# Performance work log

Measured on AMD Instinct MI355X. Metric: run time of the kernel, lower is better.

## Reference

```python
import jax, jax.numpy as jnp
import numpy as np

B, P, D, DOUT = 8, 4096, 512, 512
E, K, NHID = 8, 2, 2  # num_experts, top_k, num_mlp_hidden_layers
L = NHID + 1          # number of D->D (relu) layers per expert


def setup_inputs() -> dict:
    key = jax.random.key(0)
    ks = jax.random.split(key, 7)
    s_in = 1.0 / np.sqrt(D)
    s_g = 1.0 / np.sqrt(3.0)
    x = jax.random.normal(ks[0], (B, P, D), dtype=jnp.float32)
    Wg = jax.random.uniform(ks[1], (3, E), jnp.float32, -s_g, s_g)
    bg = jax.random.uniform(ks[2], (E,), jnp.float32, -s_g, s_g)
    Wh = jax.random.uniform(ks[3], (E, L, D, D), jnp.float32, -s_in, s_in)
    bh = jax.random.uniform(ks[4], (E, L, D), jnp.float32, -s_in, s_in)
    Wo = jax.random.uniform(ks[5], (E, D, DOUT), jnp.float32, -s_in, s_in)
    bo = jax.random.uniform(ks[6], (E, DOUT), jnp.float32, -s_in, s_in)
    return {"x": x, "Wg": Wg, "bg": bg, "Wh": Wh, "bh": bh, "Wo": Wo, "bo": bo}


def _moe_forward(x, Wg, bg, Wh, bh, Wo, bo):
    b, p, d = x.shape
    xf = x.reshape(-1, d)                       # [N, D]
    n = xf.shape[0]
    gates = xf[:, -3:] @ Wg + bg                # [N, E] (eval mode: no noise)
    topv, topi = jax.lax.top_k(gates, K)        # [N, K]
    topw = jax.nn.softmax(topv, axis=-1)        # [N, K]
    # scatter top-k softmax weights into dense [N, E] mask
    mask = jnp.zeros_like(gates).at[jnp.arange(n)[:, None], topi].set(topw)
    out = jnp.zeros((n, Wo.shape[-1]), dtype=xf.dtype)
    for e in range(E):  # fixed small expert loop; zero-weight rows contribute 0
        h = xf
        for l in range(L):
            h = jax.nn.relu(h @ Wh[e, l] + bh[e, l])
        y = h @ Wo[e] + bo[e]
        out = out + mask[:, e:e + 1] * y
    return out.reshape(b, p, -1)


def reference(x, Wg, bg, Wh, bh, Wo, bo):
    return _moe_forward(x, Wg, bg, Wh, bh, Wo, bo)
```

## Files before the change

### kernel.cpp

```cpp
#include <hip/hip_runtime.h>
#include <cstdint>
#include <cstddef>

#define DD   512
#define NTOK 32768
#define NE   8
#define BM   128
#define BN   128
#define BK   32
#define NT   (DD / BK)
#define RBLK 1024

typedef unsigned int  u32;
typedef unsigned short u16;
typedef unsigned long long u64;
using f16x8 = __attribute__((ext_vector_type(8))) _Float16;
using f32x4 = __attribute__((ext_vector_type(4))) float;

#define OA 0
#define OB 4096

__device__ __forceinline__ u16 f16bits(float f) {
    union { _Float16 h; u16 u; } p;
    p.h = (_Float16)f;
    return p.u;
}
__device__ __forceinline__ uint4 pack_f16x8(const float4& a, const float4& b) {
    uint4 r;
    r.x = (u32)f16bits(a.x) | ((u32)f16bits(a.y) << 16);
    r.y = (u32)f16bits(a.z) | ((u32)f16bits(a.w) << 16);
    r.z = (u32)f16bits(b.x) | ((u32)f16bits(b.y) << 16);
    r.w = (u32)f16bits(b.z) | ((u32)f16bits(b.w) << 16);
    return r;
}

__device__ __forceinline__ void gl16(const void* src, const u16* ldsdst) {
    __builtin_amdgcn_global_load_lds(
        (const __attribute__((address_space(1))) u32*)src,
        (__attribute__((address_space(3))) u32*)(void*)ldsdst, 16, 0, 0);
}

__global__ __launch_bounds__(RBLK) void route_kernel(
    const float* __restrict__ x,
    const float* __restrict__ Wg,
    const float* __restrict__ bg,
    int t0, int T,
    int* __restrict__ counts,
    int* __restrict__ eids,
    float* __restrict__ wts) {
    __shared__ int lcnt[NE];
    int tid = threadIdx.x;
    if (tid < NE) lcnt[tid] = 0;
    __syncthreads();

    int i = blockIdx.x * RBLK + tid;
    bool active = (i < T);
    int e0 = 0, e1 = 0;
    if (active) {
        int n = t0 + i;
        const float* xr = x + (size_t)n * DD + (DD - 3);
        float x0 = xr[0], x1 = xr[1], x2 = xr[2];
        float g[NE];
#pragma unroll
        for (int e = 0; e < NE; e++)
            g[e] = x0 * Wg[e] + x1 * Wg[NE + e] + x2 * Wg[2 * NE + e] + bg[e];
        float v0 = g[0];
#pragma unroll
        for (int e = 1; e < NE; e++) if (g[e] > v0) { v0 = g[e]; e0 = e; }
        float v1 = -3.0e38f; e1 = -1;
#pragma unroll
        for (int e = 0; e < NE; e++) if (e != e0 && g[e] > v1) { v1 = g[e]; e1 = e; }
        float t = expf(v1 - v0);
        float s = 1.0f / (1.0f + t);
        eids[2 * i] = e0; eids[2 * i + 1] = e1;
        wts[2 * i] = s;  wts[2 * i + 1] = t * s;
    }

    int lane = tid & 63;
#pragma unroll
    for (int k = 0; k < 2; k++) {
        int e = active ? (k ? e1 : e0) : -1;
#pragma unroll
        for (int ex = 0; ex < NE; ex++) {
            u64 m = __ballot(e == ex);
            if (m && lane == 0) atomicAdd(&lcnt[ex], __popcll(m));
        }
    }
    __syncthreads();
    if (tid < NE && lcnt[tid]) atomicAdd(&counts[tid], lcnt[tid]);
}

__global__ void offsets_kernel(const int* __restrict__ counts,
                               int* __restrict__ off,
                               int* __restrict__ cursor) {
    if (threadIdx.x == 0) {
        int acc = 0;
        for (int e = 0; e < NE; e++) {
            off[e] = acc;
            cursor[e] = acc;
            acc += (counts[e] + (BM - 1)) & ~(BM - 1);
        }
        off[NE] = acc;
    }
}

__global__ __launch_bounds__(RBLK) void scatter_kernel(
    int t0, int T,
    const int* __restrict__ eids,
    int* __restrict__ cursor,
    int* __restrict__ list_token,
    int* __restrict__ posl) {
    __shared__ int lcnt[NE], lbase[NE];
    __shared__ int woff[RBLK / 64][NE];
    int tid = threadIdx.x, lane = tid & 63, wv = tid >> 6;
    int i = blockIdx.x * RBLK + tid;
    bool active = (i < T);
    u64 lmask = (1ull << lane) - 1ull;

#pragma unroll
    for (int k = 0; k < 2; k++) {
        if (tid < NE) lcnt[tid] = 0;
        __syncthreads();
        int e = active ? eids[2 * i + k] : -1;
        u64 mymask = 0;
#pragma unroll
        for (int ex = 0; ex < NE; ex++) {
            u64 m = __ballot(e == ex);
            if (e == ex) mymask = m;
            if (m && lane == 0) woff[wv][ex] = atomicAdd(&lcnt[ex], __popcll(m));
        }
        __syncthreads();
        if (tid < NE) lbase[tid] = lcnt[tid] ? atomicAdd(&cursor[tid], lcnt[tid]) : 0;
        __syncthreads();
        if (active) {
            int p = lbase[e] + woff[wv][e] + __popcll(mymask & lmask);
            list_token[p] = t0 + i;
            posl[2 * i + k] = p;
        }
        __syncthreads();
    }
}

__global__ void convert_w(const float* __restrict__ Wh,
                          const float* __restrict__ Wo,
                          u16* __restrict__ Wt) {
    __shared__ float tile[32][33];
    int z = blockIdx.z;
    int e = z >> 2, l = z & 3;
    const float* src = (l < 3) ? (Wh + ((size_t)e * 3 + l) * DD * DD)
                               : (Wo + (size_t)e * DD * DD);
    int bx = blockIdx.x, by = blockIdx.y;
    int tx = threadIdx.x, ty = threadIdx.y;
#pragma unroll
    for (int j = 0; j < 4; j++)
        tile[ty + j * 8][tx] = src[(size_t)(by * 32 + ty + j * 8) * DD + bx * 32 + tx];
    __syncthreads();
    u16* d = Wt + (size_t)z * DD * DD;
#pragma unroll
    for (int j = 0; j < 4; j++) {
        int n = bx * 32 + ty + j * 8;
        int k = by * 32 + tx;
        d[(size_t)n * DD + k] = f16bits(tile[tx][ty + j * 8]);
    }
}

template <bool GATHER, bool RELU, bool OUTF32>
__global__ __launch_bounds__(256, 3) void moe_gemm(
    const float* __restrict__ Xf,
    const u16* __restrict__ Ain,
    const int* __restrict__ list_token,
    const u16* __restrict__ Wt,
    int layer,
    const float* __restrict__ bptr, int bestride,
    const int* __restrict__ off,
    u16* __restrict__ Ch,
    float* __restrict__ Cf)
{
    u32 nb = gridDim.x, qq = nb >> 3, bid = blockIdx.x;
    u32 wg = (bid & 7) * qq + (bid >> 3);
    int rb = (int)(wg >> 2) * BM;
    if (rb >= off[NE]) return;
    int cb = (int)(wg & 3) * BN;
    int e = 0;
#pragma unroll
    for (int s = 1; s < NE; s++) if (rb >= off[s]) e = s;

    __shared__ u16 lds[8192];

    const int tid = threadIdx.x;
    const int lane = tid & 63, wv = tid >> 6;

    int rowj[2], usj[2];
#pragma unroll
    for (int j = 0; j < 2; j++) {
        rowj[j] = j * 64 + (tid >> 2);
        usj[j]  = (tid & 3) ^ ((rowj[j] >> 1) & 3);
    }

    const size_t wbase = ((size_t)e * 4 + layer) * (size_t)DD * DD;
    const u16* bS[2];
    const u16* aS[2];
    const float* aF[2];
    int tokj[2] = {0, 0};
#pragma unroll
    for (int j = 0; j < 2; j++) {
        bS[j] = Wt + wbase + (size_t)(cb + rowj[j]) * DD + usj[j] * 8;
        if (GATHER) {
            tokj[j] = list_token[rb + rowj[j]];
            aF[j] = Xf + (size_t)(tokj[j] < 0 ? 0 : tokj[j]) * DD + usj[j] * 8;
        } else {
            aS[j] = Ain + (size_t)(rb + rowj[j]) * DD + usj[j] * 8;
        }
    }
    const int cb8[2] = { wv * 512, 2048 + wv * 512 };

    const int r15 = lane & 15, lg = lane >> 4;
    const int wr = (wv >> 1) * 64, wc = (wv & 1) * 64;
    u32 aoff[4], boff[4];
#pragma unroll
    for (int i = 0; i < 4; i++) {
        int ar = wr + i * 16 + r15;
        aoff[i] = (u32)(ar * 32 + (lg ^ ((ar >> 1) & 3)) * 8);
        int br = wc + i * 16 + r15;
        boff[i] = (u32)(br * 32 + (lg ^ ((br >> 1) & 3)) * 8);
    }

    f32x4 acc[4][4];
#pragma unroll
    for (int i = 0; i < 4; i++)
#pragma unroll
        for (int j = 0; j < 4; j++) acc[i][j] = (f32x4){0.f, 0.f, 0.f, 0.f};

    for (int t = 0; t < NT; t++) {
        const int k0 = t * BK;
#pragma unroll
        for (int j = 0; j < 2; j++)
            gl16(bS[j] + k0, &lds[OB + cb8[j]]);
        if (GATHER) {
#pragma unroll
            for (int j = 0; j < 2; j++) {
                const float4* fp = (const float4*)(aF[j] + k0);
                float4 f0 = fp[0], f1 = fp[1];
                if (tokj[j] < 0) { f0 = make_float4(0.f, 0.f, 0.f, 0.f); f1 = f0; }
                *(uint4*)&lds[OA + rowj[j] * 32 + (tid & 3) * 8] = pack_f16x8(f0, f1);
            }
        } else {
#pragma unroll
            for (int j = 0; j < 2; j++)
                gl16(aS[j] + k0, &lds[OA + cb8[j]]);
        }
        __syncthreads();

        f16x8 a[4];
#pragma unroll
        for (int mi = 0; mi < 4; mi++)
            a[mi] = *(const f16x8*)&lds[OA + aoff[mi]];
#pragma unroll
        for (int ni = 0; ni < 4; ni++) {
            f16x8 b = *(const f16x8*)&lds[OB + boff[ni]];
#pragma unroll
            for (int mi = 0; mi < 4; mi++)
                acc[mi][ni] = __builtin_amdgcn_mfma_f32_16x16x32_f16(a[mi], b, acc[mi][ni], 0, 0, 0);
        }
        __syncthreads();
    }

#pragma unroll
    for (int ni = 0; ni < 4; ni++) {
        int col = cb + wc + ni * 16 + r15;
        float bbias = bptr[e * bestride + col];
#pragma unroll
        for (int mi = 0; mi < 4; mi++) {
            int row0 = rb + wr + mi * 16 + lg * 4;
#pragma unroll
            for (int rr = 0; rr < 4; rr++) {
                float v = acc[mi][ni][rr] + bbias;
                if (RELU) v = fmaxf(v, 0.f);
                size_t idx = (size_t)(row0 + rr) * DD + col;
                if (OUTF32) Cf[idx] = v;
                else        Ch[idx] = f16bits(v);
            }
        }
    }
}

__global__ void combine_kernel(int t0, int T,
                               const float* __restrict__ y,
                               const int* __restrict__ posl,
                               const float* __restrict__ wts,
                               float* __restrict__ out) {
    int idx = blockIdx.x * blockDim.x + threadIdx.x;
    if (idx >= T * (DD / 4)) return;
    int i = idx >> 7;
    int j = idx & 127;
    int p0 = posl[2 * i], p1 = posl[2 * i + 1];
    float w0 = wts[2 * i], w1 = wts[2 * i + 1];
    float4 a = ((const float4*)(y + (size_t)p0 * DD))[j];
    float4 b = ((const float4*)(y + (size_t)p1 * DD))[j];
    float4 c;
    c.x = w0 * a.x + w1 * b.x;
    c.y = w0 * a.y + w1 * b.y;
    c.z = w0 * a.z + w1 * b.z;
    c.w = w0 * a.w + w1 * b.w;
    ((float4*)(out + (size_t)(t0 + i) * DD))[j] = c;
}

extern "C" void kernel_launch(void* const* d_in, const int* in_sizes, int n_in,
                              void* d_out, int out_size, void* d_ws, size_t ws_size,
                              hipStream_t stream) {
    const float* x  = (const float*)d_in[0];
    const float* Wg = (const float*)d_in[1];
    const float* bg = (const float*)d_in[2];
    const float* Wh = (const float*)d_in[3];
    const float* bh = (const float*)d_in[4];
    const float* Wo = (const float*)d_in[5];
    const float* bo = (const float*)d_in[6];
    float* out = (float*)d_out;

    const size_t WT_ELEMS = (size_t)NE * 4 * DD * DD;
    int T = NTOK;
    while (T > 64) {
        size_t C = 2 * (size_t)T + NE * BM;
        size_t need = 4096 + WT_ELEMS * 2 + 3 * ((size_t)T * 2 * 4)
                    + C * 4 + 512
                    + C * (size_t)DD * 2
                    + C * (size_t)DD * 4;
        if (need <= ws_size) break;
        T >>= 1;
    }
    int phases = (NTOK + T - 1) / T;
    size_t C = 2 * (size_t)T + NE * BM;

    char* p = (char*)d_ws;
    int* counts = (int*)p;
    int* off    = (int*)(p + 64);
    int* cursor = (int*)(p + 128);
    char* q = p + 4096;
    u16* Wt = (u16*)q;    q += WT_ELEMS * 2;
    int* eids = (int*)q;  q += (size_t)T * 2 * 4;
    int* posl = (int*)q;  q += (size_t)T * 2 * 4;
    float* wts = (float*)q; q += (size_t)T * 2 * 4;
    int* list_token = (int*)q; q += C * 4;
    q = (char*)(((uintptr_t)q + 255) & ~(uintptr_t)255);
    u16* bufA = (u16*)q;  q += C * DD * 2;
    u16* bufB = (u16*)q;
    float* yf = (float*)bufB;

    convert_w<<<dim3(16, 16, 32), dim3(32, 8), 0, stream>>>(Wh, Wo, Wt);

    for (int ph = 0; ph < phases; ph++) {
        int t0 = ph * T;
        int Tc = (NTOK - t0 < T) ? (NTOK - t0) : T;

        hipMemsetAsync(counts, 0, 256, stream);
        hipMemsetAsync(list_token, 0xFF, C * 4, stream);

        route_kernel<<<(Tc + RBLK - 1) / RBLK, RBLK, 0, stream>>>(
            x, Wg, bg, t0, Tc, counts, eids, wts);
        offsets_kernel<<<1, 64, 0, stream>>>(counts, off, cursor);
        scatter_kernel<<<(Tc + RBLK - 1) / RBLK, RBLK, 0, stream>>>(
            t0, Tc, eids, cursor, list_token, posl);

        unsigned NB = (unsigned)(C / BM) * (DD / BN);
        moe_gemm<true, true, false><<<NB, 256, 0, stream>>>(
            x, nullptr, list_token, Wt, 0,
            bh, 3 * DD, off, bufA, nullptr);
        moe_gemm<false, true, false><<<NB, 256, 0, stream>>>(
            nullptr, bufA, nullptr, Wt, 1,
            bh + DD, 3 * DD, off, bufB, nullptr);
        moe_gemm<false, true, false><<<NB, 256, 0, stream>>>(
            nullptr, bufB, nullptr, Wt, 2,
            bh + 2 * DD, 3 * DD, off, bufA, nullptr);
        moe_gemm<false, false, true><<<NB, 256, 0, stream>>>(
            nullptr, bufA, nullptr, Wt, 3,
            bo, DD, off, nullptr, yf);

        combine_kernel<<<((size_t)Tc * (DD / 4) + 255) / 256, 256, 0, stream>>>(
            t0, Tc, yf, posl, wts, out);
    }
}
```

Baseline: 296.3 us.

## Fuse four expert MLP layers into one kernel keeping activations in LDS

Replaces the four per-layer grouped GEMM launches with a single fused_mlp kernel. Each block holds a 128x512 fp16 activation tile in LDS and runs all four layers on it, streaming weights directly from global memory into registers. This removes the intermediate activation round-trips through HBM and three kernel launches. It also drops the phased workspace sizing, always processing all tokens at once, and stores the final expert output as fp16 rather than fp32, halving combine reads. The costs are 128KB of LDS per block, which caps occupancy, weight operands read from global with no LDS reuse across waves, a full-size workspace assumption, and reduced output precision.

```diff
diff --git a/kernel.cpp b/kernel.cpp
--- a/kernel.cpp
+++ b/kernel.cpp
@@ -6,10 +6,9 @@
 #define NTOK 32768
 #define NE   8
 #define BM   128
-#define BN   128
-#define BK   32
-#define NT   (DD / BK)
 #define RBLK 1024
+#define CMAX (2 * NTOK + NE * BM)
+#define PMAX (CMAX / BM)
 
 typedef unsigned int  u32;
 typedef unsigned short u16;
@@ -17,13 +16,15 @@
 using f16x8 = __attribute__((ext_vector_type(8))) _Float16;
 using f32x4 = __attribute__((ext_vector_type(4))) float;
 
-#define OA 0
-#define OB 4096
-
 __device__ __forceinline__ u16 f16bits(float f) {
     union { _Float16 h; u16 u; } p;
     p.h = (_Float16)f;
     return p.u;
+}
+__device__ __forceinline__ float h2f(u16 v) {
+    union { _Float16 h; u16 u; } p;
+    p.u = v;
+    return (float)p.h;
 }
 __device__ __forceinline__ uint4 pack_f16x8(const float4& a, const float4& b) {
     uint4 r;
@@ -34,17 +35,10 @@
     return r;
 }
 
-__device__ __forceinline__ void gl16(const void* src, const u16* ldsdst) {
-    __builtin_amdgcn_global_load_lds(
-        (const __attribute__((address_space(1))) u32*)src,
-        (__attribute__((address_space(3))) u32*)(void*)ldsdst, 16, 0, 0);
-}
-
 __global__ __launch_bounds__(RBLK) void route_kernel(
     const float* __restrict__ x,
     const float* __restrict__ Wg,
     const float* __restrict__ bg,
-    int t0, int T,
     int* __restrict__ counts,
     int* __restrict__ eids,
     float* __restrict__ wts) {
@@ -54,11 +48,10 @@
     __syncthreads();
 
     int i = blockIdx.x * RBLK + tid;
-    bool active = (i < T);
+    bool active = (i < NTOK);
     int e0 = 0, e1 = 0;
     if (active) {
-        int n = t0 + i;
-        const float* xr = x + (size_t)n * DD + (DD - 3);
+        const float* xr = x + (size_t)i * DD + (DD - 3);
         float x0 = xr[0], x1 = xr[1], x2 = xr[2];
         float g[NE];
 #pragma unroll
@@ -105,7 +98,6 @@
 }
 
 __global__ __launch_bounds__(RBLK) void scatter_kernel(
-    int t0, int T,
     const int* __restrict__ eids,
     int* __restrict__ cursor,
     int* __restrict__ list_token,
@@ -114,7 +106,7 @@
     __shared__ int woff[RBLK / 64][NE];
     int tid = threadIdx.x, lane = tid & 63, wv = tid >> 6;
     int i = blockIdx.x * RBLK + tid;
-    bool active = (i < T);
+    bool active = (i < NTOK);
     u64 lmask = (1ull << lane) - 1ull;
 
 #pragma unroll
@@ -134,7 +126,7 @@
         __syncthreads();
         if (active) {
             int p = lbase[e] + woff[wv][e] + __popcll(mymask & lmask);
-            list_token[p] = t0 + i;
+            list_token[p] = i;
             posl[2 * i + k] = p;
         }
         __syncthreads();
@@ -164,145 +156,131 @@
     }
 }
 
-template <bool GATHER, bool RELU, bool OUTF32>
-__global__ __launch_bounds__(256, 3) void moe_gemm(
-    const float* __restrict__ Xf,
-    const u16* __restrict__ Ain,
+__global__ __launch_bounds__(512, 2) void fused_mlp(
+    const float* __restrict__ x,
     const int* __restrict__ list_token,
     const u16* __restrict__ Wt,
-    int layer,
-    const float* __restrict__ bptr, int bestride,
-    const int* __restrict__ off,
-    u16* __restrict__ Ch,
-    float* __restrict__ Cf)
+    const float* __restrict__ bh,
+    const float* __restrict__ bo,
+    const int* __restrict__ ctrl,
+    u16* __restrict__ bY)
 {
-    u32 nb = gridDim.x, qq = nb >> 3, bid = blockIdx.x;
-    u32 wg = (bid & 7) * qq + (bid >> 3);
-    int rb = (int)(wg >> 2) * BM;
+    __shared__ u16 A[BM * DD];
+    const int* off = ctrl + 8;
+    const int rb = blockIdx.x * BM;
     if (rb >= off[NE]) return;
-    int cb = (int)(wg & 3) * BN;
     int e = 0;
 #pragma unroll
     for (int s = 1; s < NE; s++) if (rb >= off[s]) e = s;
-
-    __shared__ u16 lds[8192];
 
     const int tid = threadIdx.x;
     const int lane = tid & 63, wv = tid >> 6;
-
-    int rowj[2], usj[2];
-#pragma unroll
-    for (int j = 0; j < 2; j++) {
-        rowj[j] = j * 64 + (tid >> 2);
-        usj[j]  = (tid & 3) ^ ((rowj[j] >> 1) & 3);
-    }
-
-    const size_t wbase = ((size_t)e * 4 + layer) * (size_t)DD * DD;
-    const u16* bS[2];
-    const u16* aS[2];
-    const float* aF[2];
-    int tokj[2] = {0, 0};
-#pragma unroll
-    for (int j = 0; j < 2; j++) {
-        bS[j] = Wt + wbase + (size_t)(cb + rowj[j]) * DD + usj[j] * 8;
-        if (GATHER) {
-            tokj[j] = list_token[rb + rowj[j]];
-            aF[j] = Xf + (size_t)(tokj[j] < 0 ? 0 : tokj[j]) * DD + usj[j] * 8;
-        } else {
-            aS[j] = Ain + (size_t)(rb + rowj[j]) * DD + usj[j] * 8;
-        }
-    }
-    const int cb8[2] = { wv * 512, 2048 + wv * 512 };
-
     const int r15 = lane & 15, lg = lane >> 4;
-    const int wr = (wv >> 1) * 64, wc = (wv & 1) * 64;
-    u32 aoff[4], boff[4];
-#pragma unroll
-    for (int i = 0; i < 4; i++) {
-        int ar = wr + i * 16 + r15;
-        aoff[i] = (u32)(ar * 32 + (lg ^ ((ar >> 1) & 3)) * 8);
-        int br = wc + i * 16 + r15;
-        boff[i] = (u32)(br * 32 + (lg ^ ((br >> 1) & 3)) * 8);
-    }
-
-    f32x4 acc[4][4];
-#pragma unroll
-    for (int i = 0; i < 4; i++)
-#pragma unroll
-        for (int j = 0; j < 4; j++) acc[i][j] = (f32x4){0.f, 0.f, 0.f, 0.f};
-
-    for (int t = 0; t < NT; t++) {
-        const int k0 = t * BK;
-#pragma unroll
-        for (int j = 0; j < 2; j++)
-            gl16(bS[j] + k0, &lds[OB + cb8[j]]);
-        if (GATHER) {
-#pragma unroll
-            for (int j = 0; j < 2; j++) {
-                const float4* fp = (const float4*)(aF[j] + k0);
-                float4 f0 = fp[0], f1 = fp[1];
-                if (tokj[j] < 0) { f0 = make_float4(0.f, 0.f, 0.f, 0.f); f1 = f0; }
-                *(uint4*)&lds[OA + rowj[j] * 32 + (tid & 3) * 8] = pack_f16x8(f0, f1);
+
+    {
+        int row = tid >> 2, q = tid & 3;
+        int tok = list_token[rb + row];
+        const float* xr = x + (size_t)(tok < 0 ? 0 : tok) * DD;
+#pragma unroll
+        for (int c8 = 0; c8 < 16; c8++) {
+            int u = q * 16 + c8;
+            float4 f0 = make_float4(0.f, 0.f, 0.f, 0.f), f1 = f0;
+            if (tok >= 0) {
+                f0 = *(const float4*)(xr + u * 8);
+                f1 = *(const float4*)(xr + u * 8 + 4);
             }
-        } else {
-#pragma unroll
-            for (int j = 0; j < 2; j++)
-                gl16(aS[j] + k0, &lds[OA + cb8[j]]);
-        }
-        __syncthreads();
-
-        f16x8 a[4];
-#pragma unroll
-        for (int mi = 0; mi < 4; mi++)
-            a[mi] = *(const f16x8*)&lds[OA + aoff[mi]];
+            *(uint4*)&A[row * DD + ((u ^ (row & 7)) << 3)] = pack_f16x8(f0, f1);
+        }
+    }
+    __syncthreads();
+
+    int colc[4];
+#pragma unroll
+    for (int ni = 0; ni < 4; ni++) colc[ni] = wv * 64 + ni * 16 + r15;
+
+    for (int l = 0; l < 4; l++) {
+        const u16* W = Wt + (size_t)(e * 4 + l) * DD * DD;
+        const float* bias = (l < 3) ? (bh + (size_t)(e * 3 + l) * DD)
+                                    : (bo + (size_t)e * DD);
+        const u16* bp[4];
+#pragma unroll
+        for (int ni = 0; ni < 4; ni++)
+            bp[ni] = W + (size_t)colc[ni] * DD + lg * 8;
+
+        f32x4 acc[8][4];
+#pragma unroll
+        for (int mi = 0; mi < 8; mi++)
+#pragma unroll
+            for (int ni = 0; ni < 4; ni++) acc[mi][ni] = (f32x4){0.f, 0.f, 0.f, 0.f};
+
+        f16x8 Bn[4];
+#pragma unroll
+        for (int ni = 0; ni < 4; ni++) Bn[ni] = *(const f16x8*)(bp[ni]);
+#pragma unroll
+        for (int t = 0; t < 16; t++) {
+            f16x8 Bc[4];
+#pragma unroll
+            for (int ni = 0; ni < 4; ni++) Bc[ni] = Bn[ni];
+            if (t < 15) {
+#pragma unroll
+                for (int ni = 0; ni < 4; ni++)
+                    Bn[ni] = *(const f16x8*)(bp[ni] + (t + 1) * 32);
+            }
+            f16x8 Af[8];
+#pragma unroll
+            for (int mi = 0; mi < 8; mi++) {
+                int row = mi * 16 + r15;
+                Af[mi] = *(const f16x8*)&A[row * DD + ((((t << 2) + lg) ^ (row & 7)) << 3)];
+            }
+#pragma unroll
+            for (int ni = 0; ni < 4; ni++)
+#pragma unroll
+                for (int mi = 0; mi < 8; mi++)
+                    acc[mi][ni] = __builtin_amdgcn_mfma_f32_16x16x32_f16(Af[mi], Bc[ni], acc[mi][ni], 0, 0, 0);
+        }
+        __syncthreads();
+
 #pragma unroll
         for (int ni = 0; ni < 4; ni++) {
-            f16x8 b = *(const f16x8*)&lds[OB + boff[ni]];
-#pragma unroll
-            for (int mi = 0; mi < 4; mi++)
-                acc[mi][ni] = __builtin_amdgcn_mfma_f32_16x16x32_f16(a[mi], b, acc[mi][ni], 0, 0, 0);
-        }
-        __syncthreads();
-    }
-
-#pragma unroll
-    for (int ni = 0; ni < 4; ni++) {
-        int col = cb + wc + ni * 16 + r15;
-        float bbias = bptr[e * bestride + col];
-#pragma unroll
-        for (int mi = 0; mi < 4; mi++) {
-            int row0 = rb + wr + mi * 16 + lg * 4;
-#pragma unroll
-            for (int rr = 0; rr < 4; rr++) {
-                float v = acc[mi][ni][rr] + bbias;
-                if (RELU) v = fmaxf(v, 0.f);
-                size_t idx = (size_t)(row0 + rr) * DD + col;
-                if (OUTF32) Cf[idx] = v;
-                else        Ch[idx] = f16bits(v);
+            int col = colc[ni];
+            float bb = bias[col];
+#pragma unroll
+            for (int mi = 0; mi < 8; mi++) {
+#pragma unroll
+                for (int rr = 0; rr < 4; rr++) {
+                    int row = mi * 16 + lg * 4 + rr;
+                    float v = acc[mi][ni][rr] + bb;
+                    if (l < 3) {
+                        v = fmaxf(v, 0.f);
+                        A[row * DD + (((col >> 3) ^ (row & 7)) << 3) + (col & 7)] = f16bits(v);
+                    } else {
+                        bY[(size_t)(rb + row) * DD + col] = f16bits(v);
+                    }
+                }
             }
         }
-    }
-}
-
-__global__ void combine_kernel(int t0, int T,
-                               const float* __restrict__ y,
+        if (l < 3) __syncthreads();
+    }
+}
+
+__global__ void combine_kernel(const u16* __restrict__ y,
                                const int* __restrict__ posl,
                                const float* __restrict__ wts,
                                float* __restrict__ out) {
     int idx = blockIdx.x * blockDim.x + threadIdx.x;
-    if (idx >= T * (DD / 4)) return;
+    if (idx >= NTOK * (DD / 4)) return;
     int i = idx >> 7;
     int j = idx & 127;
     int p0 = posl[2 * i], p1 = posl[2 * i + 1];
     float w0 = wts[2 * i], w1 = wts[2 * i + 1];
-    float4 a = ((const float4*)(y + (size_t)p0 * DD))[j];
-    float4 b = ((const float4*)(y + (size_t)p1 * DD))[j];
+    ushort4 a = ((const ushort4*)(y + (size_t)p0 * DD))[j];
+    ushort4 b = ((const ushort4*)(y + (size_t)p1 * DD))[j];
     float4 c;
-    c.x = w0 * a.x + w1 * b.x;
-    c.y = w0 * a.y + w1 * b.y;
-    c.z = w0 * a.z + w1 * b.z;
-    c.w = w0 * a.w + w1 * b.w;
-    ((float4*)(out + (size_t)(t0 + i) * DD))[j] = c;
+    c.x = w0 * h2f(a.x) + w1 * h2f(b.x);
+    c.y = w0 * h2f(a.y) + w1 * h2f(b.y);
+    c.z = w0 * h2f(a.z) + w1 * h2f(b.z);
+    c.w = w0 * h2f(a.w) + w1 * h2f(b.w);
+    ((float4*)(out + (size_t)i * DD))[j] = c;
 }
 
 extern "C" void kernel_launch(void* const* d_in, const int* in_sizes, int n_in,
@@ -317,65 +295,32 @@
     const float* bo = (const float*)d_in[6];
     float* out = (float*)d_out;
 
-    const size_t WT_ELEMS = (size_t)NE * 4 * DD * DD;
-    int T = NTOK;
-    while (T > 64) {
-        size_t C = 2 * (size_t)T + NE * BM;
-        size_t need = 4096 + WT_ELEMS * 2 + 3 * ((size_t)T * 2 * 4)
-                    + C * 4 + 512
-                    + C * (size_t)DD * 2
-                    + C * (size_t)DD * 4;
-        if (need <= ws_size) break;
-        T >>= 1;
-    }
-    int phases = (NTOK + T - 1) / T;
-    size_t C = 2 * (size_t)T + NE * BM;
-
     char* p = (char*)d_ws;
-    int* counts = (int*)p;
-    int* off    = (int*)(p + 64);
-    int* cursor = (int*)(p + 128);
+    int* ctrl   = (int*)p;
+    int* counts = ctrl;
+    int* off    = ctrl + 8;
+    int* cursor = ctrl + 17;
     char* q = p + 4096;
-    u16* Wt = (u16*)q;    q += WT_ELEMS * 2;
-    int* eids = (int*)q;  q += (size_t)T * 2 * 4;
-    int* posl = (int*)q;  q += (size_t)T * 2 * 4;
-    float* wts = (float*)q; q += (size_t)T * 2 * 4;
-    int* list_token = (int*)q; q += C * 4;
+    u16* Wt = (u16*)q;      q += (size_t)NE * 4 * DD * DD * 2;
+    int* eids = (int*)q;    q += (size_t)NTOK * 2 * 4;
+    int* posl = (int*)q;    q += (size_t)NTOK * 2 * 4;
+    float* wts = (float*)q; q += (size_t)NTOK * 2 * 4;
+    int* list_token = (int*)q; q += (size_t)CMAX * 4;
     q = (char*)(((uintptr_t)q + 255) & ~(uintptr_t)255);
-    u16* bufA = (u16*)q;  q += C * DD * 2;
-    u16* bufB = (u16*)q;
-    float* yf = (float*)bufB;
+    u16* bY = (u16*)q;
+
+    hipMemsetAsync(ctrl, 0, 4096, stream);
+    hipMemsetAsync(list_token, 0xFF, (size_t)CMAX * 4, stream);
 
     convert_w<<<dim3(16, 16, 32), dim3(32, 8), 0, stream>>>(Wh, Wo, Wt);
-
-    for (int ph = 0; ph < phases; ph++) {
-        int t0 = ph * T;
-        int Tc = (NTOK - t0 < T) ? (NTOK - t0) : T;
-
-        hipMemsetAsync(counts, 0, 256, stream);
-        hipMemsetAsync(list_token, 0xFF, C * 4, stream);
-
-        route_kernel<<<(Tc + RBLK - 1) / RBLK, RBLK, 0, stream>>>(
-            x, Wg, bg, t0, Tc, counts, eids, wts);
-        offsets_kernel<<<1, 64, 0, stream>>>(counts, off, cursor);
-        scatter_kernel<<<(Tc + RBLK - 1) / RBLK, RBLK, 0, stream>>>(
-            t0, Tc, eids, cursor, list_token, posl);
-
-        unsigned NB = (unsigned)(C / BM) * (DD / BN);
-        moe_gemm<true, true, false><<<NB, 256, 0, stream>>>(
-            x, nullptr, list_token, Wt, 0,
-            bh, 3 * DD, off, bufA, nullptr);
-        moe_gemm<false, true, false><<<NB, 256, 0, stream>>>(
-            nullptr, bufA, nullptr, Wt, 1,
-            bh + DD, 3 * DD, off, bufB, nullptr);
-        moe_gemm<false, true, false><<<NB, 256, 0, stream>>>(
-            nullptr, bufB, nullptr, Wt, 2,
-            bh + 2 * DD, 3 * DD, off, bufA, nullptr);
-        moe_gemm<false, false, true><<<NB, 256, 0, stream>>>(
-            nullptr, bufA, nullptr, Wt, 3,
-            bo, DD, off, nullptr, yf);
-
-        combine_kernel<<<((size_t)Tc * (DD / 4) + 255) / 256, 256, 0, stream>>>(
-            t0, Tc, yf, posl, wts, out);
-    }
-}
+    route_kernel<<<(NTOK + RBLK - 1) / RBLK, RBLK, 0, stream>>>(
+        x, Wg, bg, counts, eids, wts);
+    offsets_kernel<<<1, 64, 0, stream>>>(counts, off, cursor);
+    scatter_kernel<<<(NTOK + RBLK - 1) / RBLK, RBLK, 0, stream>>>(
+        eids, cursor, list_token, posl);
+
+    fused_mlp<<<PMAX, 512, 0, stream>>>(x, list_token, Wt, bh, bo, ctrl, bY);
+
+    combine_kernel<<<(NTOK * (DD / 4) + 255) / 256, 256, 0, stream>>>(
+        bY, posl, wts, out);
+}
```

Measured after the change: 770.2 us. 160% more time.
